# Kernel optimization log

Hardware: AMD Instinct MI355X
Metric: run time of the kernel (lower is better)

## Reference

```python
import jax, jax.numpy as jnp
import numpy as np

B, N = 32, 256            # batch, nodes (square cost matrix)
EMB, H, DQK, FF, L = 256, 16, 16, 512, 5
EPS = 1e-5


def _heads(x):
    # [B, N, H*DQK] -> [B, H, N, DQK]
    b, n, _ = x.shape
    return x.reshape(b, n, H, DQK).transpose(0, 2, 1, 3)


def _inorm(x, g, b):
    # InstanceNorm1d over node axis per (batch, channel); affine per channel
    m = x.mean(axis=1, keepdims=True)
    v = x.var(axis=1, keepdims=True)
    return (x - m) * jax.lax.rsqrt(v + EPS) * g + b


def _block(x_row, x_col, cost, p):
    Wq, Ws, Wa, Wv, Wc, bc, g1, be1, W1, bf1, W2, bf2, g2, be2 = p
    q = _heads(x_row @ Wq)
    k_s = _heads(x_row @ Ws)
    k_a = _heads(x_col @ Wa)
    v = _heads(x_col @ Wv)
    # mixed score: dot-product scores + additive cost-matrix bias, pre-softmax
    scores = (jnp.einsum('bhid,bhjd->bhij', q, k_a)
              + jnp.einsum('bhid,bhjd->bhij', q, k_s)) * (1.0 / np.sqrt(DQK).astype(np.float32))
    scores = scores + cost[:, None, :, :]
    att = jax.nn.softmax(scores, axis=-1)
    out = jnp.einsum('bhij,bhjd->bhid', att, v)          # [B,H,N,DQK]
    out = out.transpose(0, 2, 1, 3).reshape(x_row.shape[0], -1, H * DQK)
    mh = out @ Wc + bc
    o1 = _inorm(x_row + mh, g1, be1)
    ff = jax.nn.relu(o1 @ W1 + bf1) @ W2 + bf2
    return _inorm(o1 + ff, g2, be2)


def _encoder(row, col, cost, params):
    cost_t = cost.transpose(0, 2, 1)
    for l in range(L):  # fixed small layer loop
        pr = tuple(t[l, 0] for t in params)
        pc = tuple(t[l, 1] for t in params)
        row_new = _block(row, col, cost, pr)
        col_new = _block(col, row, cost_t, pc)
        row, col = row_new, col_new
    return row, col


def setup_inputs() -> dict:
    key = jax.random.key(0)
    ks = jax.random.split(key, 16)
    sc_e = 1.0 / np.sqrt(EMB)
    sc_h = 1.0 / np.sqrt(H * DQK)
    sc_f = 1.0 / np.sqrt(FF)
    inp = {
        'row_emb': jax.random.normal(ks[0], (B, N, EMB), jnp.float32),
        'col_emb': jax.random.normal(ks[1], (B, N, EMB), jnp.float32),
        'cost_mat': jax.random.uniform(ks[2], (B, N, N), jnp.float32),
        # stacked params: leading dims [L, 2] = (layer, row/col block)
        'Wq': jax.random.normal(ks[3], (L, 2, EMB, H * DQK), jnp.float32) * sc_e,
        'Ws': jax.random.normal(ks[4], (L, 2, EMB, H * DQK), jnp.float32) * sc_e,
        'Wa': jax.random.normal(ks[5], (L, 2, EMB, H * DQK), jnp.float32) * sc_e,
        'Wv': jax.random.normal(ks[6], (L, 2, EMB, H * DQK), jnp.float32) * sc_e,
        'Wc': jax.random.normal(ks[7], (L, 2, H * DQK, EMB), jnp.float32) * sc_h,
        'bc': jnp.zeros((L, 2, EMB), jnp.float32),
        'g1': jnp.ones((L, 2, EMB), jnp.float32),
        'be1': jnp.zeros((L, 2, EMB), jnp.float32),
        'W1': jax.random.normal(ks[8], (L, 2, EMB, FF), jnp.float32) * sc_e,
        'bf1': jnp.zeros((L, 2, FF), jnp.float32),
        'W2': jax.random.normal(ks[9], (L, 2, FF, EMB), jnp.float32) * sc_f,
        'bf2': jnp.zeros((L, 2, EMB), jnp.float32),
        'g2': jnp.ones((L, 2, EMB), jnp.float32),
        'be2': jnp.zeros((L, 2, EMB), jnp.float32),
    }
    return inp


def reference(row_emb, col_emb, cost_mat, Wq, Ws, Wa, Wv, Wc, bc, g1, be1,
              W1, bf1, W2, bf2, g2, be2):
    params = (Wq, Ws, Wa, Wv, Wc, bc, g1, be1, W1, bf1, W2, bf2, g2, be2)
    return _encoder(row_emb, col_emb, cost_mat, params)
```

## Files before the change

### kernel.cpp

```cpp
#include <hip/hip_runtime.h>
#include <cstddef>
#include <cstdint>

#define EMB 256
#define NN  256
#define BB  32
#define FFD 512
#define LL  5
#define MTOT (BB*NN)

typedef unsigned short u16;
typedef _Float16 f16;
typedef f16   f16x8 __attribute__((ext_vector_type(8)));
typedef float f32x4 __attribute__((ext_vector_type(4)));

static const size_t MB = 1048576ull;
static const size_t PLX = 2097152;
static const size_t PLH = 4194304;
static const size_t FRAG = 4194304;
static const size_t WSEG = 589824;
#define OQ 0
#define OS 65536
#define OA 131072
#define OV 196608
#define OC 262144
#define O1 327680
#define O2 458752

__device__ __forceinline__ float f16_f(u16 u) {
    union { u16 u; f16 f; } c; c.u = u;
    return (float)c.f;
}
__device__ __forceinline__ u16 f16_u(f16 h) {
    union { f16 f; u16 u; } c; c.f = h;
    return c.u;
}
__device__ __forceinline__ void split2h(float x, u16& hi, u16& lo) {
    f16 h = (f16)x;
    f16 l = (f16)(x - (float)h);
    hi = f16_u(h); lo = f16_u(l);
}

__device__ __forceinline__ void gll16(const void* g, void* l) {
    __builtin_amdgcn_global_load_lds(
        (const __attribute__((address_space(1))) unsigned int*)g,
        (__attribute__((address_space(3))) unsigned int*)l,
        16, 0, 0);
}

template<typename PF>
__device__ __forceinline__ void mfma_core2(f32x4 (&acc)[4][4], int nsp, int K,
                                           int m0, int n0,
                                           u16* AsH, u16* AsL, u16* BsH, PF pf)
{
    const int tid  = threadIdx.x;
    const int lane = tid & 63;
    const int w    = tid >> 6;
    const int wr   = w >> 1, wc = w & 1;
    const int l15  = lane & 15, lg = lane >> 4;

    for (int p = 0; p < nsp; ++p) {
        const u16 *Ah, *Al, *Bh;
        pf(p, Ah, Al, Bh);
        const int nkt = K >> 6;
        for (int kt = 0; kt < nkt; ++kt) {
            __syncthreads();
            #pragma unroll
            for (int c = 0; c < 4; ++c) {
                int slot = w * 256 + c * 64 + lane;
                int row  = slot >> 3;
                int cc   = slot & 7;
                int kc   = cc ^ (row & 7);
                const size_t ga = (size_t)(m0 + row) * K + (kt << 6) + kc * 8;
                const size_t gb = (size_t)(n0 + row) * K + (kt << 6) + kc * 8;
                const int lo = (w * 256 + c * 64) * 8;
                gll16(Ah + ga, AsH + lo);
                gll16(Al + ga, AsL + lo);
                gll16(Bh + gb, BsH + lo);
            }
            __syncthreads();
            #pragma unroll
            for (int ks = 0; ks < 2; ++ks) {
                f16x8 ah[4], al[4], bh[4];
                #pragma unroll
                for (int i = 0; i < 4; ++i) {
                    int arow = wr * 64 + i * 16 + l15;
                    int aoff = ((arow << 3) + ((ks * 4 + lg) ^ (arow & 7))) * 8;
                    ah[i] = *(const f16x8*)(AsH + aoff);
                    al[i] = *(const f16x8*)(AsL + aoff);
                    int brow = wc * 64 + i * 16 + l15;
                    int boff = ((brow << 3) + ((ks * 4 + lg) ^ (brow & 7))) * 8;
                    bh[i] = *(const f16x8*)(BsH + boff);
                }
                #pragma unroll
                for (int mi = 0; mi < 4; ++mi)
                    #pragma unroll
                    for (int ni = 0; ni < 4; ++ni) {
                        acc[mi][ni] = __builtin_amdgcn_mfma_f32_16x16x32_f16(
                            ah[mi], bh[ni], acc[mi][ni], 0, 0, 0);
                        acc[mi][ni] = __builtin_amdgcn_mfma_f32_16x16x32_f16(
                            al[mi], bh[ni], acc[mi][ni], 0, 0, 0);
                    }
            }
        }
    }
}

__global__ __launch_bounds__(256)
void qkv_k(const u16* __restrict__ Ssp, const u16* __restrict__ wt,
           u16* __restrict__ Qf, u16* __restrict__ Kf, u16* __restrict__ Vf)
{
    const int s   = blockIdx.z;
    const int seg = blockIdx.y >> 1;
    const int n0  = (blockIdx.y & 1) * 128;
    const int m0  = blockIdx.x * 128;

    const u16* Xsh = Ssp + (size_t)s * (2 * PLX);
    const u16* Xsl = Xsh + PLX;
    const u16* Xoh = Ssp + (size_t)(1 - s) * (2 * PLX);
    const u16* Xol = Xoh + PLX;
    const u16* Wh  = wt + (size_t)s * (2 * WSEG);
    const int  nsp = (seg == 1) ? 2 : 1;

    __shared__ u16 AsH[8192], AsL[8192], BsH[8192];

    f32x4 acc[4][4];
    #pragma unroll
    for (int i = 0; i < 4; ++i)
        #pragma unroll
        for (int j = 0; j < 4; ++j) acc[i][j] = (f32x4){0.f, 0.f, 0.f, 0.f};

    auto pf = [&](int p, const u16*& Ah, const u16*& Al, const u16*& Bh) {
        if (seg == 0)      { Ah = Xsh; Al = Xsl; Bh = Wh + OQ; }
        else if (seg == 2) { Ah = Xoh; Al = Xol; Bh = Wh + OV; }
        else if (p == 0)   { Ah = Xsh; Al = Xsl; Bh = Wh + OS; }
        else               { Ah = Xoh; Al = Xol; Bh = Wh + OA; }
    };
    mfma_core2(acc, nsp, 256, m0, n0, AsH, AsL, BsH, pf);

    const int lane = threadIdx.x & 63, w = threadIdx.x >> 6;
    const int wr = w >> 1, wc = w & 1, l15 = lane & 15, lg = lane >> 4;

    u16* Of = ((seg == 0) ? Qf : (seg == 1) ? Kf : Vf) + (size_t)s * FRAG;

    #pragma unroll
    for (int mi = 0; mi < 4; ++mi)
        #pragma unroll
        for (int ni = 0; ni < 4; ++ni) {
            const int col = n0 + wc * 64 + ni * 16 + l15;
            #pragma unroll
            for (int r = 0; r < 4; ++r) {
                const int row = m0 + wr * 64 + mi * 16 + lg * 4 + r;
                const int bloc = row >> 8;
                const int h = col >> 4;
                if (seg == 0) {
                    const int T = (row >> 4) & 15, rq = row & 15;
                    const int half = (col >> 3) & 1, e = col & 7;
                    const size_t base = (((size_t)bloc * 16 + T) * 16 + h) * 512
                                      + half * 128 + rq * 8 + e;
                    Of[base] = f16_u((f16)acc[mi][ni][r]);
                } else if (seg == 1) {
                    const int g = (row >> 5) & 7, jj = row & 31;
                    const int t = (jj >> 2) & 1;
                    const int lk = ((jj >> 3) << 2) | (jj & 3);
                    const int half = (col >> 3) & 1, e = col & 7;
                    const size_t base = (((size_t)bloc * 8 + g) * 16 + h) * 1024
                                      + t * 512 + half * 128 + lk * 8 + e;
                    u16 hi, lo; split2h(acc[mi][ni][r], hi, lo);
                    Of[base] = hi;
                    Of[base + 256] = lo;
                } else {
                    const int g = (row >> 5) & 7, jj = row & 31;
                    const int lgv = jj >> 3, e = jj & 7;
                    const int lv = col & 15;
                    const size_t base = (((size_t)bloc * 8 + g) * 16 + h) * 1024
                                      + (lgv * 16 + lv) * 8 + e;
                    Of[base] = f16_u((f16)acc[mi][ni][r]);
                }
            }
        }
}

template<int RESID, int RELU, int OUTF32, int OUTF16>
__global__ __launch_bounds__(256)
void gemm3(const u16* __restrict__ Asp, size_t AMK, int K,
           const u16* __restrict__ wt, int boff,
           const float* __restrict__ bias, int Nd,
           const u16* __restrict__ Rsp, const float* __restrict__ Rf,
           float* __restrict__ Of, u16* __restrict__ Ob, size_t OMN, int l)
{
    const int s  = blockIdx.z;
    const int n0 = blockIdx.y * 128;
    const int m0 = blockIdx.x * 128;

    const u16* Ah0 = Asp + (size_t)s * (2 * AMK);
    const u16* Al0 = Ah0 + AMK;
    const u16* Bh0 = wt + (size_t)s * (2 * WSEG) + boff;

    __shared__ u16 AsH[8192], AsL[8192], BsH[8192];

    f32x4 acc[4][4];
    #pragma unroll
    for (int i = 0; i < 4; ++i)
        #pragma unroll
        for (int j = 0; j < 4; ++j) acc[i][j] = (f32x4){0.f, 0.f, 0.f, 0.f};

    auto pf = [&](int p, const u16*& Ah, const u16*& Al, const u16*& Bh) {
        Ah = Ah0; Al = Al0; Bh = Bh0;
    };
    mfma_core2(acc, 1, K, m0, n0, AsH, AsL, BsH, pf);

    const float* bs = bias + (size_t)(l * 2 + s) * Nd;
    const int lane = threadIdx.x & 63, w = threadIdx.x >> 6;
    const int wr = w >> 1, wc = w & 1, l15 = lane & 15, lg = lane >> 4;

    #pragma unroll
    for (int mi = 0; mi < 4; ++mi)
        #pragma unroll
        for (int ni = 0; ni < 4; ++ni) {
            const int col = n0 + wc * 64 + ni * 16 + l15;
            const float bv = bs[col];
            #pragma unroll
            for (int r = 0; r < 4; ++r) {
                const int row = m0 + wr * 64 + mi * 16 + lg * 4 + r;
                const size_t idx = (size_t)row * Nd + col;
                float v = acc[mi][ni][r] + bv;
                if constexpr (RESID == 1) {
                    v += Rf[(size_t)s * PLX + idx];
                } else if constexpr (RESID == 2) {
                    const u16* Rh = Rsp + (size_t)s * (2 * PLX);
                    v += f16_f(Rh[idx]) + f16_f(Rh[PLX + idx]);
                }
                if constexpr (RELU) v = fmaxf(v, 0.f);
                if constexpr (OUTF32) Of[(size_t)s * PLX + idx] = v;
                if constexpr (OUTF16) {
                    u16 hi, lo; split2h(v, hi, lo);
                    u16* Oh = Ob + (size_t)s * (2 * OMN);
                    Oh[idx] = hi;
                    Oh[OMN + idx] = lo;
                }
            }
        }
}

__global__ __launch_bounds__(512)
void attn_k(const u16* __restrict__ Qf, const u16* __restrict__ Kf,
            const u16* __restrict__ Vf, const float* __restrict__ cost,
            u16* __restrict__ AOs)
{
    const int id = blockIdx.x;
    const int bs = id & 63;
    const int ib = id >> 6;
    const int b = bs >> 1, s = bs & 1;
    const int i0 = ib * 32;

    const int tid = threadIdx.x;
    const int lane = tid & 63;
    const int wv = tid >> 6;
    const int l15 = lane & 15, lg = lane >> 4;
    const int h0 = wv * 2;

    const u16* Qfs = Qf + (size_t)s * FRAG;
    const u16* Kfs = Kf + (size_t)s * FRAG;
    const u16* Vfs = Vf + (size_t)s * FRAG;
    const float* cb = cost + (size_t)b * NN * NN;

    __shared__ float Cs[2][32][36];

    f16x8 qb1[2][2];
    #pragma unroll
    for (int hh = 0; hh < 2; ++hh)
        #pragma unroll
        for (int it = 0; it < 2; ++it) {
            const int T = (i0 >> 4) + it;
            const size_t base = (((size_t)b * 16 + T) * 16 + (h0 + hh)) * 512
                              + (lg & 1) * 128 + l15 * 8;
            qb1[hh][it] = *(const f16x8*)(Qfs + base);
        }

    float m_s[2][2], l_s[2][2];
    f32x4 occ[2][2];
    #pragma unroll
    for (int hh = 0; hh < 2; ++hh)
        #pragma unroll
        for (int it = 0; it < 2; ++it) {
            m_s[hh][it] = -1e30f;
            l_s[hh][it] = 0.f;
            occ[hh][it] = (f32x4){0.f, 0.f, 0.f, 0.f};
        }

    auto stageCost = [&](int g, int buf) {
        if (tid < 256) {
            if (s == 0) {
                const int i = tid >> 3, j4 = (tid & 7) * 4;
                float4 cv = *(const float4*)(cb + (size_t)(i0 + i) * NN + g * 32 + j4);
                Cs[buf][i][j4+0] = cv.x; Cs[buf][i][j4+1] = cv.y;
                Cs[buf][i][j4+2] = cv.z; Cs[buf][i][j4+3] = cv.w;
            } else {
                const int j = tid >> 3, i4 = (tid & 7) * 4;
                float4 cv = *(const float4*)(cb + (size_t)(g * 32 + j) * NN + i0 + i4);
                Cs[buf][i4+0][j] = cv.x; Cs[buf][i4+1][j] = cv.y;
                Cs[buf][i4+2][j] = cv.z; Cs[buf][i4+3][j] = cv.w;
            }
        }
    };

    auto loadKV = [&](int g, f16x8 (&kA)[2][2], f16x8 (&vv)[2]) {
        #pragma unroll
        for (int hh = 0; hh < 2; ++hh) {
            const size_t kb = (((size_t)b * 8 + g) * 16 + (h0 + hh)) * 1024;
            kA[hh][0] = *(const f16x8*)(Kfs + kb + lane * 8);
            kA[hh][1] = *(const f16x8*)(Kfs + kb + 512 + lane * 8);
            vv[hh]    = *(const f16x8*)(Vfs + kb + lane * 8);
        }
    };

    f16x8 kA0[2][2], vv0[2], kA1[2][2], vv1[2];
    stageCost(0, 0);
    loadKV(0, kA0, vv0);
    __syncthreads();

    auto iter = [&](int g, int cur,
                    f16x8 (&kAc)[2][2], f16x8 (&vvc)[2],
                    f16x8 (&kAn)[2][2], f16x8 (&vvn)[2]) {
        if (g < 7) {
            stageCost(g + 1, cur ^ 1);
            loadKV(g + 1, kAn, vvn);
        }
        float cst[2][8];
        #pragma unroll
        for (int it = 0; it < 2; ++it)
            #pragma unroll
            for (int t = 0; t < 2; ++t) {
                float4 cv = *(const float4*)&Cs[cur][it * 16 + l15][8 * lg + 4 * t];
                cst[it][t*4+0] = cv.x; cst[it][t*4+1] = cv.y;
                cst[it][t*4+2] = cv.z; cst[it][t*4+3] = cv.w;
            }
        #pragma unroll
        for (int hh = 0; hh < 2; ++hh) {
            #pragma unroll
            for (int it = 0; it < 2; ++it) {
                f32x4 st0 = (f32x4){0.f,0.f,0.f,0.f};
                f32x4 st1 = (f32x4){0.f,0.f,0.f,0.f};
                st0 = __builtin_amdgcn_mfma_f32_16x16x32_f16(kAc[hh][0], qb1[hh][it], st0, 0,0,0);
                st1 = __builtin_amdgcn_mfma_f32_16x16x32_f16(kAc[hh][1], qb1[hh][it], st1, 0,0,0);

                float sv[8];
                #pragma unroll
                for (int r = 0; r < 4; ++r) {
                    sv[r]     = st0[r] * 0.25f + cst[it][r];
                    sv[4 + r] = st1[r] * 0.25f + cst[it][4 + r];
                }
                float tm = sv[0];
                #pragma unroll
                for (int e = 1; e < 8; ++e) tm = fmaxf(tm, sv[e]);
                tm = fmaxf(tm, __shfl_xor(tm, 16));
                tm = fmaxf(tm, __shfl_xor(tm, 32));

                const float mo = m_s[hh][it];
                const float mn = fmaxf(mo, tm);
                const float sc = __expf(mo - mn);
                float p[8], ts = 0.f;
                #pragma unroll
                for (int e = 0; e < 8; ++e) { p[e] = __expf(sv[e] - mn); ts += p[e]; }
                ts += __shfl_xor(ts, 16);
                ts += __shfl_xor(ts, 32);
                l_s[hh][it] = l_s[hh][it] * sc + ts;
                m_s[hh][it] = mn;

                f32x4 o = occ[hh][it];
                o[0] *= sc; o[1] *= sc; o[2] *= sc; o[3] *= sc;
                f16x8 pb;
                #pragma unroll
                for (int e = 0; e < 8; ++e) pb[e] = (f16)p[e];
                o = __builtin_amdgcn_mfma_f32_16x16x32_f16(vvc[hh], pb, o, 0,0,0);
                occ[hh][it] = o;
            }
        }
        __syncthreads();
    };

    for (int gp = 0; gp < 8; gp += 2) {
        iter(gp,     0, kA0, vv0, kA1, vv1);
        iter(gp + 1, 1, kA1, vv1, kA0, vv0);
    }

    u16* AOh = AOs + (size_t)s * (2 * PLX);
    u16* AOl = AOh + PLX;
    #pragma unroll
    for (int hh = 0; hh < 2; ++hh)
        #pragma unroll
        for (int it = 0; it < 2; ++it) {
            const float inv = 1.f / l_s[hh][it];
            const size_t base = (size_t)(b * NN + i0 + it * 16 + l15) * EMB
                              + (h0 + hh) * 16 + lg * 4;
            ushort4 vh4, vl4;
            u16 h_, l_;
            split2h(occ[hh][it][0] * inv, h_, l_); vh4.x = h_; vl4.x = l_;
            split2h(occ[hh][it][1] * inv, h_, l_); vh4.y = h_; vl4.y = l_;
            split2h(occ[hh][it][2] * inv, h_, l_); vh4.z = h_; vl4.z = l_;
            split2h(occ[hh][it][3] * inv, h_, l_); vh4.w = h_; vl4.w = l_;
            *(ushort4*)(AOh + base) = vh4;
            *(ushort4*)(AOl + base) = vl4;
        }
}

template<int WF32>
__global__ __launch_bounds__(256)
void inorm_k(const float* __restrict__ Xb,
             const float* __restrict__ gb, const float* __restrict__ bb,
             float* __restrict__ Yf, u16* __restrict__ Ysp, int l)
{
    const int bx = blockIdx.x;
    const int b = bx >> 2, cg = bx & 3;
    const int s = blockIdx.y;
    const float* X = Xb + (size_t)s * PLX + (size_t)b * NN * EMB;
    const int tid = threadIdx.x;
    const int cl = tid & 63, q = tid >> 6;
    const int c = cg * 64 + cl;

    float sum = 0.f, ss = 0.f;
    for (int n = q * 64; n < q * 64 + 64; ++n) {
        float x = X[(size_t)n * EMB + c];
        sum += x; ss += x * x;
    }
    __shared__ float Ssum[4][64], Sss[4][64], Sa[64], Sb2[64];
    Ssum[q][cl] = sum; Sss[q][cl] = ss;
    __syncthreads();
    if (q == 0) {
        float s4 = Ssum[0][cl] + Ssum[1][cl] + Ssum[2][cl] + Ssum[3][cl];
        float q4 = Sss[0][cl] + Sss[1][cl] + Sss[2][cl] + Sss[3][cl];
        float mean = s4 * (1.f / NN);
        float var  = q4 * (1.f / NN) - mean * mean;
        float inv  = rsqrtf(var + 1e-5f);
        float gv = gb[(size_t)(l * 2 + s) * EMB + c];
        float bv = bb[(size_t)(l * 2 + s) * EMB + c];
        float a = gv * inv;
        Sa[cl]  = a;
        Sb2[cl] = bv - mean * a;
    }
    __syncthreads();
    const float a = Sa[cl], b2 = Sb2[cl];
    u16* Yh = Ysp + (size_t)s * (2 * PLX) + (size_t)b * NN * EMB;
    u16* Yl = Yh + PLX;
    float* Yo = WF32 ? (Yf + (size_t)s * PLX + (size_t)b * NN * EMB) : nullptr;
    for (int n = q * 64; n < q * 64 + 64; ++n) {
        const size_t idx = (size_t)n * EMB + c;
        float y = X[idx] * a + b2;
        if constexpr (WF32) Yo[idx] = y;
        u16 hi, lo; split2h(y, hi, lo);
        Yh[idx] = hi; Yl[idx] = lo;
    }
}

__global__ __launch_bounds__(256)
void conv0_k(const float* __restrict__ rowe, const float* __restrict__ cole,
             u16* __restrict__ S0)
{
    const int side = blockIdx.y;
    const float* src = side ? cole : rowe;
    const size_t o = ((size_t)blockIdx.x * 256 + threadIdx.x) * 4;
    float4 v = *(const float4*)(src + o);
    u16 h0,l0,h1,l1,h2,l2,h3,l3;
    split2h(v.x, h0, l0); split2h(v.y, h1, l1);
    split2h(v.z, h2, l2); split2h(v.w, h3, l3);
    u16* Sh = S0 + (size_t)side * (2 * PLX);
    u16* Sl = Sh + PLX;
    ushort4 vh; vh.x=h0; vh.y=h1; vh.z=h2; vh.w=h3;
    ushort4 vl; vl.x=l0; vl.y=l1; vl.z=l2; vl.w=l3;
    *(ushort4*)(Sh + o) = vh;
    *(ushort4*)(Sl + o) = vl;
}

__global__ __launch_bounds__(256)
void wconv_k(const float* __restrict__ Wq, const float* __restrict__ Ws,
             const float* __restrict__ Wa, const float* __restrict__ Wv,
             const float* __restrict__ Wc, const float* __restrict__ W1,
             const float* __restrict__ W2, u16* __restrict__ wt, int l)
{
    const int t = blockIdx.x;
    const int s = blockIdx.y;
    const float* src; int Kd, Nd, tr, tc; size_t dsto;
    if (t < 80) {
        int m = t >> 4, tt = t & 15; tr = tt >> 2; tc = tt & 3; Kd = 256; Nd = 256;
        const float* w0;
        switch (m) {
            case 0: w0 = Wq; dsto = OQ; break;
            case 1: w0 = Ws; dsto = OS; break;
            case 2: w0 = Wa; dsto = OA; break;
            case 3: w0 = Wv; dsto = OV; break;
            default: w0 = Wc; dsto = OC; break;
        }
        src = w0 + (size_t)(l * 2 + s) * 65536;
    } else if (t < 112) {
        int tt = t - 80; tr = tt >> 3; tc = tt & 7; Kd = 256; Nd = 512;
        src = W1 + (size_t)(l * 2 + s) * 131072; dsto = O1;
    } else {
        int tt = t - 112; tr = tt >> 2; tc = tt & 3; Kd = 512; Nd = 256;
        src = W2 + (size_t)(l * 2 + s) * 131072; dsto = O2;
    }
    const int k0 = tr * 64, n0 = tc * 64;
    __shared__ float T[64][65];
    const int tid = threadIdx.x;
    {
        const int j4 = tid & 15, i0 = tid >> 4;
        #pragma unroll
        for (int ii = 0; ii < 4; ++ii) {
            int i = ii * 16 + i0;
            float4 v = *(const float4*)(src + (size_t)(k0 + i) * Nd + n0 + j4 * 4);
            T[i][j4*4+0] = v.x; T[i][j4*4+1] = v.y;
            T[i][j4*4+2] = v.z; T[i][j4*4+3] = v.w;
        }
    }
    __syncthreads();
    u16* Whi = wt + (size_t)s * (2 * WSEG) + dsto;
    {
        const int k4 = tid & 15, j0 = tid >> 4;
        #pragma unroll
        for (int jj = 0; jj < 4; ++jj) {
            int j = jj * 16 + j0;
            int n = n0 + j;
            ushort4 vh;
            vh.x = f16_u((f16)T[k4*4+0][j]);
            vh.y = f16_u((f16)T[k4*4+1][j]);
            vh.z = f16_u((f16)T[k4*4+2][j]);
            vh.w = f16_u((f16)T[k4*4+3][j]);
            *(ushort4*)(Whi + (size_t)n * Kd + k0 + k4 * 4) = vh;
        }
    }
}

extern "C" void kernel_launch(void* const* d_in, const int* in_sizes, int n_in,
                              void* d_out, int out_size, void* d_ws, size_t ws_size,
                              hipStream_t stream)
{
    const float* row_emb = (const float*)d_in[0];
    const float* col_emb = (const float*)d_in[1];
    const float* cost    = (const float*)d_in[2];
    const float* Wq  = (const float*)d_in[3];
    const float* Ws  = (const float*)d_in[4];
    const float* Wa  = (const float*)d_in[5];
    const float* Wv  = (const float*)d_in[6];
    const float* Wc  = (const float*)d_in[7];
    const float* bc  = (const float*)d_in[8];
    const float* g1  = (const float*)d_in[9];
    const float* be1 = (const float*)d_in[10];
    const float* W1  = (const float*)d_in[11];
    const float* bf1 = (const float*)d_in[12];
    const float* W2  = (const float*)d_in[13];
    const float* bf2 = (const float*)d_in[14];
    const float* g2  = (const float*)d_in[15];
    const float* be2 = (const float*)d_in[16];

    char* W = (char*)d_ws;
    u16*   Sb[2]  = { (u16*)(W + 0 * MB), (u16*)(W + 16 * MB) };
    u16*   Qf     = (u16*)(W + 32 * MB);
    u16*   Kf     = (u16*)(W + 48 * MB);
    u16*   Vf     = (u16*)(W + 64 * MB);
    u16*   wt     = (u16*)(W + 80 * MB);
    u16*   AOsp   = (u16*)(W + 96 * MB);
    u16*   o1sp   = (u16*)(W + 32 * MB);
    float* y1f    = (float*)(W + 48 * MB);
    float* o1f    = (float*)(W + 64 * MB);
    u16*   hsp    = (u16*)(W + 96 * MB);
    float* y2f    = (float*)(W + 48 * MB);

    conv0_k<<<dim3(2048, 2), 256, 0, stream>>>(row_emb, col_emb, Sb[0]);

    for (int l = 0; l < LL; ++l) {
        const int cur = l & 1;

        wconv_k<<<dim3(144, 2), 256, 0, stream>>>(Wq, Ws, Wa, Wv, Wc, W1, W2, wt, l);

        qkv_k<<<dim3(MTOT / 128, 6, 2), 256, 0, stream>>>(Sb[cur], wt, Qf, Kf, Vf);

        attn_k<<<dim3(512), 512, 0, stream>>>(Qf, Kf, Vf, cost, AOsp);

        gemm3<2, 0, 1, 0><<<dim3(MTOT / 128, 2, 2), 256, 0, stream>>>(
            AOsp, PLX, 256, wt, OC, bc, 256, Sb[cur], nullptr, y1f, nullptr, 0, l);

        inorm_k<1><<<dim3(BB * 4, 2), 256, 0, stream>>>(y1f, g1, be1, o1f, o1sp, l);

        gemm3<0, 1, 0, 1><<<dim3(MTOT / 128, 4, 2), 256, 0, stream>>>(
            o1sp, PLX, 256, wt, O1, bf1, 512, nullptr, nullptr, nullptr, hsp, PLH, l);

        gemm3<1, 0, 1, 0><<<dim3(MTOT / 128, 2, 2), 256, 0, stream>>>(
            hsp, PLH, 512, wt, O2, bf2, 256, nullptr, o1f, y2f, nullptr, 0, l);

        if (l == LL - 1)
            inorm_k<1><<<dim3(BB * 4, 2), 256, 0, stream>>>(y2f, g2, be2,
                (float*)d_out, Sb[1 - cur], l);
        else
            inorm_k<0><<<dim3(BB * 4, 2), 256, 0, stream>>>(y2f, g2, be2,
                nullptr, Sb[1 - cur], l);
    }
    (void)in_sizes; (void)n_in; (void)out_size; (void)ws_size;
}
```

Baseline: 897.8 us.

## Hoist weight conversion out of layer loop and use 128x64 tiles for dense GEMMs

Weight transposition/conversion to fp16 now runs once for all layers and sides in a single launch, with per-layer segments indexed by layer in the GEMM kernels. The shared MFMA core is templated on the N tile width, and the output-projection and feed-forward GEMMs switch to 128x64 tiles with four waves stacked along M. This doubles the block count of those launches to better fill the GPU and removes four kernel launches. The cost is a larger weight workspace and less B-tile reuse per block.

Measured after the change: 860.9 us. 1.04x faster.

```diff
diff --git a/kernel.cpp b/kernel.cpp
--- a/kernel.cpp
+++ b/kernel.cpp
@@ -48,15 +48,17 @@
         16, 0, 0);
 }
 
-template<typename PF>
-__device__ __forceinline__ void mfma_core2(f32x4 (&acc)[4][4], int nsp, int K,
-                                           int m0, int n0,
+template<int BN, typename PF>
+__device__ __forceinline__ void mfma_core2(f32x4 (&acc)[BN/32][4], int nsp,
+                                           int K, int m0, int n0,
                                            u16* AsH, u16* AsL, u16* BsH, PF pf)
 {
+    constexpr int MI = BN / 32;
     const int tid  = threadIdx.x;
     const int lane = tid & 63;
     const int w    = tid >> 6;
-    const int wr   = w >> 1, wc = w & 1;
+    const int wr   = (BN == 128) ? (w >> 1) : w;
+    const int wc   = (BN == 128) ? (w & 1) : 0;
     const int l15  = lane & 15, lg = lane >> 4;
 
     for (int p = 0; p < nsp; ++p) {
@@ -72,28 +74,38 @@
                 int cc   = slot & 7;
                 int kc   = cc ^ (row & 7);
                 const size_t ga = (size_t)(m0 + row) * K + (kt << 6) + kc * 8;
-                const size_t gb = (size_t)(n0 + row) * K + (kt << 6) + kc * 8;
-                const int lo = (w * 256 + c * 64) * 8;
+                const int lo = slot * 8;
                 gll16(Ah + ga, AsH + lo);
                 gll16(Al + ga, AsL + lo);
-                gll16(Bh + gb, BsH + lo);
+            }
+            #pragma unroll
+            for (int c = 0; c < BN / 32; ++c) {
+                int slot = w * (BN * 2) + c * 64 + lane;
+                int row  = slot >> 3;
+                int cc   = slot & 7;
+                int kc   = cc ^ (row & 7);
+                const size_t gb = (size_t)(n0 + row) * K + (kt << 6) + kc * 8;
+                gll16(Bh + gb, BsH + slot * 8);
             }
             __syncthreads();
             #pragma unroll
             for (int ks = 0; ks < 2; ++ks) {
-                f16x8 ah[4], al[4], bh[4];
+                f16x8 ah[MI], al[MI], bh[4];
                 #pragma unroll
-                for (int i = 0; i < 4; ++i) {
-                    int arow = wr * 64 + i * 16 + l15;
+                for (int i = 0; i < MI; ++i) {
+                    int arow = wr * (MI * 16) + i * 16 + l15;
                     int aoff = ((arow << 3) + ((ks * 4 + lg) ^ (arow & 7))) * 8;
                     ah[i] = *(const f16x8*)(AsH + aoff);
                     al[i] = *(const f16x8*)(AsL + aoff);
+                }
+                #pragma unroll
+                for (int i = 0; i < 4; ++i) {
                     int brow = wc * 64 + i * 16 + l15;
                     int boff = ((brow << 3) + ((ks * 4 + lg) ^ (brow & 7))) * 8;
                     bh[i] = *(const f16x8*)(BsH + boff);
                 }
                 #pragma unroll
-                for (int mi = 0; mi < 4; ++mi)
+                for (int mi = 0; mi < MI; ++mi)
                     #pragma unroll
                     for (int ni = 0; ni < 4; ++ni) {
                         acc[mi][ni] = __builtin_amdgcn_mfma_f32_16x16x32_f16(
@@ -108,7 +120,8 @@
 
 __global__ __launch_bounds__(256)
 void qkv_k(const u16* __restrict__ Ssp, const u16* __restrict__ wt,
-           u16* __restrict__ Qf, u16* __restrict__ Kf, u16* __restrict__ Vf)
+           u16* __restrict__ Qf, u16* __restrict__ Kf, u16* __restrict__ Vf,
+           int l)
 {
     const int s   = blockIdx.z;
     const int seg = blockIdx.y >> 1;
@@ -119,7 +132,7 @@
     const u16* Xsl = Xsh + PLX;
     const u16* Xoh = Ssp + (size_t)(1 - s) * (2 * PLX);
     const u16* Xol = Xoh + PLX;
-    const u16* Wh  = wt + (size_t)s * (2 * WSEG);
+    const u16* Wh  = wt + (size_t)(l * 2 + s) * WSEG;
     const int  nsp = (seg == 1) ? 2 : 1;
 
     __shared__ u16 AsH[8192], AsL[8192], BsH[8192];
@@ -136,7 +149,7 @@
         else if (p == 0)   { Ah = Xsh; Al = Xsl; Bh = Wh + OS; }
         else               { Ah = Xoh; Al = Xol; Bh = Wh + OA; }
     };
-    mfma_core2(acc, nsp, 256, m0, n0, AsH, AsL, BsH, pf);
+    mfma_core2<128>(acc, nsp, 256, m0, n0, AsH, AsL, BsH, pf);
 
     const int lane = threadIdx.x & 63, w = threadIdx.x >> 6;
     const int wr = w >> 1, wc = w & 1, l15 = lane & 15, lg = lane >> 4;
@@ -181,7 +194,7 @@
         }
 }
 
-template<int RESID, int RELU, int OUTF32, int OUTF16>
+template<int BN, int RESID, int RELU, int OUTF32, int OUTF16>
 __global__ __launch_bounds__(256)
 void gemm3(const u16* __restrict__ Asp, size_t AMK, int K,
            const u16* __restrict__ wt, int boff,
@@ -189,40 +202,43 @@
            const u16* __restrict__ Rsp, const float* __restrict__ Rf,
            float* __restrict__ Of, u16* __restrict__ Ob, size_t OMN, int l)
 {
+    constexpr int MI = BN / 32;
     const int s  = blockIdx.z;
-    const int n0 = blockIdx.y * 128;
+    const int n0 = blockIdx.y * BN;
     const int m0 = blockIdx.x * 128;
 
     const u16* Ah0 = Asp + (size_t)s * (2 * AMK);
     const u16* Al0 = Ah0 + AMK;
-    const u16* Bh0 = wt + (size_t)s * (2 * WSEG) + boff;
-
-    __shared__ u16 AsH[8192], AsL[8192], BsH[8192];
-
-    f32x4 acc[4][4];
+    const u16* Bh0 = wt + (size_t)(l * 2 + s) * WSEG + boff;
+
+    __shared__ u16 AsH[8192], AsL[8192], BsH[BN * 64];
+
+    f32x4 acc[MI][4];
     #pragma unroll
-    for (int i = 0; i < 4; ++i)
+    for (int i = 0; i < MI; ++i)
         #pragma unroll
         for (int j = 0; j < 4; ++j) acc[i][j] = (f32x4){0.f, 0.f, 0.f, 0.f};
 
     auto pf = [&](int p, const u16*& Ah, const u16*& Al, const u16*& Bh) {
         Ah = Ah0; Al = Al0; Bh = Bh0;
     };
-    mfma_core2(acc, 1, K, m0, n0, AsH, AsL, BsH, pf);
+    mfma_core2<BN>(acc, 1, K, m0, n0, AsH, AsL, BsH, pf);
 
     const float* bs = bias + (size_t)(l * 2 + s) * Nd;
     const int lane = threadIdx.x & 63, w = threadIdx.x >> 6;
-    const int wr = w >> 1, wc = w & 1, l15 = lane & 15, lg = lane >> 4;
+    const int wr = (BN == 128) ? (w >> 1) : w;
+    const int wc = (BN == 128) ? (w & 1) : 0;
+    const int l15 = lane & 15, lg = lane >> 4;
 
     #pragma unroll
-    for (int mi = 0; mi < 4; ++mi)
+    for (int mi = 0; mi < MI; ++mi)
         #pragma unroll
         for (int ni = 0; ni < 4; ++ni) {
             const int col = n0 + wc * 64 + ni * 16 + l15;
             const float bv = bs[col];
             #pragma unroll
             for (int r = 0; r < 4; ++r) {
-                const int row = m0 + wr * 64 + mi * 16 + lg * 4 + r;
+                const int row = m0 + wr * (MI * 16) + mi * 16 + lg * 4 + r;
                 const size_t idx = (size_t)row * Nd + col;
                 float v = acc[mi][ni][r] + bv;
                 if constexpr (RESID == 1) {
@@ -476,10 +492,10 @@
 void wconv_k(const float* __restrict__ Wq, const float* __restrict__ Ws,
              const float* __restrict__ Wa, const float* __restrict__ Wv,
              const float* __restrict__ Wc, const float* __restrict__ W1,
-             const float* __restrict__ W2, u16* __restrict__ wt, int l)
+             const float* __restrict__ W2, u16* __restrict__ wt)
 {
     const int t = blockIdx.x;
-    const int s = blockIdx.y;
+    const int ls = blockIdx.y;
     const float* src; int Kd, Nd, tr, tc; size_t dsto;
     if (t < 80) {
         int m = t >> 4, tt = t & 15; tr = tt >> 2; tc = tt & 3; Kd = 256; Nd = 256;
@@ -491,13 +507,13 @@
             case 3: w0 = Wv; dsto = OV; break;
             default: w0 = Wc; dsto = OC; break;
         }
-        src = w0 + (size_t)(l * 2 + s) * 65536;
+        src = w0 + (size_t)ls * 65536;
     } else if (t < 112) {
         int tt = t - 80; tr = tt >> 3; tc = tt & 7; Kd = 256; Nd = 512;
-        src = W1 + (size_t)(l * 2 + s) * 131072; dsto = O1;
+        src = W1 + (size_t)ls * 131072; dsto = O1;
     } else {
         int tt = t - 112; tr = tt >> 2; tc = tt & 3; Kd = 512; Nd = 256;
-        src = W2 + (size_t)(l * 2 + s) * 131072; dsto = O2;
+        src = W2 + (size_t)ls * 131072; dsto = O2;
     }
     const int k0 = tr * 64, n0 = tc * 64;
     __shared__ float T[64][65];
@@ -513,7 +529,7 @@
         }
     }
     __syncthreads();
-    u16* Whi = wt + (size_t)s * (2 * WSEG) + dsto;
+    u16* Whi = wt + (size_t)ls * WSEG + dsto;
     {
         const int k4 = tid & 15, j0 = tid >> 4;
         #pragma unroll
@@ -566,25 +582,24 @@
     float* y2f    = (float*)(W + 48 * MB);
 
     conv0_k<<<dim3(2048, 2), 256, 0, stream>>>(row_emb, col_emb, Sb[0]);
+    wconv_k<<<dim3(144, 10), 256, 0, stream>>>(Wq, Ws, Wa, Wv, Wc, W1, W2, wt);
 
     for (int l = 0; l < LL; ++l) {
         const int cur = l & 1;
 
-        wconv_k<<<dim3(144, 2), 256, 0, stream>>>(Wq, Ws, Wa, Wv, Wc, W1, W2, wt, l);
-
-        qkv_k<<<dim3(MTOT / 128, 6, 2), 256, 0, stream>>>(Sb[cur], wt, Qf, Kf, Vf);
+        qkv_k<<<dim3(MTOT / 128, 6, 2), 256, 0, stream>>>(Sb[cur], wt, Qf, Kf, Vf, l);
 
         attn_k<<<dim3(512), 512, 0, stream>>>(Qf, Kf, Vf, cost, AOsp);
 
-        gemm3<2, 0, 1, 0><<<dim3(MTOT / 128, 2, 2), 256, 0, stream>>>(
+        gemm3<64, 2, 0, 1, 0><<<dim3(MTOT / 128, 4, 2), 256, 0, stream>>>(
             AOsp, PLX, 256, wt, OC, bc, 256, Sb[cur], nullptr, y1f, nullptr, 0, l);
 
         inorm_k<1><<<dim3(BB * 4, 2), 256, 0, stream>>>(y1f, g1, be1, o1f, o1sp, l);
 
-        gemm3<0, 1, 0, 1><<<dim3(MTOT / 128, 4, 2), 256, 0, stream>>>(
+        gemm3<64, 0, 1, 0, 1><<<dim3(MTOT / 128, 8, 2), 256, 0, stream>>>(
             o1sp, PLX, 256, wt, O1, bf1, 512, nullptr, nullptr, nullptr, hsp, PLH, l);
 
-        gemm3<1, 0, 1, 0><<<dim3(MTOT / 128, 2, 2), 256, 0, stream>>>(
+        gemm3<64, 1, 0, 1, 0><<<dim3(MTOT / 128, 4, 2), 256, 0, stream>>>(
             hsp, PLH, 512, wt, O2, bf2, 256, nullptr, o1f, y2f, nullptr, 0, l);
 
         if (l == LL - 1)
```
